# Performance work log

Measured on AMD Instinct MI355X. Metric: run time of the kernel, lower is better.

## Reference

```python
import jax, jax.numpy as jnp
import numpy as np


def setup_inputs() -> dict:
    key = jax.random.key(0)
    k1, k2, k3, k4 = jax.random.split(key, 4)
    N = 100000          # n_users + n_items nodes
    E = 1600000         # nonzeros in normalized adjacency (avg degree 16)
    D = 64              # embedding dim
    edge_row = jnp.sort(jax.random.randint(k1, (E,), 0, N, dtype=jnp.int32))
    edge_col = jax.random.randint(k2, (E,), 0, N, dtype=jnp.int32)
    edge_val = jax.random.uniform(k3, (E,), dtype=jnp.float32)
    embeds = jax.random.normal(k4, (N, D), dtype=jnp.float32)
    return {
        "edge_row": edge_row,
        "edge_col": edge_col,
        "edge_val": edge_val,
        "embeds": embeds,
        "num_nodes": N,
    }


def reference(edge_row, edge_col, edge_val, embeds, num_nodes):
    # out = A @ embeds, A given in COO: A[row[e], col[e]] = val[e]
    gathered = edge_val[:, None] * embeds[edge_col]        # [E, D]
    out = jax.ops.segment_sum(gathered, edge_row, num_segments=num_nodes)  # [N, D]
    return out
```

## Files before the change

### kernel.cpp

```cpp
#include <hip/hip_runtime.h>


#define GCN_D 64

typedef float f4 __attribute__((ext_vector_type(4)));
typedef unsigned int u32x2 __attribute__((ext_vector_type(2)));
typedef int i32x4 __attribute__((ext_vector_type(4)));
typedef float f32x4 __attribute__((ext_vector_type(4)));

__global__ __launch_bounds__(256) void prep_kernel(
    const float* __restrict__ embeds,
    unsigned char* __restrict__ ebq,
    float* __restrict__ scale,
    int quant_blocks,
    const int* __restrict__ edge_row, int* __restrict__ row_ptr, int E, int N)
{
    if ((int)blockIdx.x < quant_blocks) {
        const int t   = blockIdx.x * blockDim.x + threadIdx.x;
        const int row = t >> 3;
        if (row >= N) return;
        const int l8 = (threadIdx.x & 7) * 8;

        const f4 a = __builtin_nontemporal_load(
            (const f4*)(embeds + (size_t)row * GCN_D + l8));
        const f4 b = __builtin_nontemporal_load(
            (const f4*)(embeds + (size_t)row * GCN_D + l8 + 4));

        float m = fmaxf(fmaxf(fmaxf(fabsf(a.x), fabsf(a.y)),
                              fmaxf(fabsf(a.z), fabsf(a.w))),
                        fmaxf(fmaxf(fabsf(b.x), fabsf(b.y)),
                              fmaxf(fabsf(b.z), fabsf(b.w))));
        m = fmaxf(m, __shfl_xor(m, 1));
        m = fmaxf(m, __shfl_xor(m, 2));
        m = fmaxf(m, __shfl_xor(m, 4));

        const float inv = (m > 0.f) ? 127.f / m : 0.f;
        const int q0 = (int)rintf(fminf(fmaxf(a.x * inv, -127.f), 127.f)) + 128;
        const int q1 = (int)rintf(fminf(fmaxf(a.y * inv, -127.f), 127.f)) + 128;
        const int q2 = (int)rintf(fminf(fmaxf(a.z * inv, -127.f), 127.f)) + 128;
        const int q3 = (int)rintf(fminf(fmaxf(a.w * inv, -127.f), 127.f)) + 128;
        const int q4 = (int)rintf(fminf(fmaxf(b.x * inv, -127.f), 127.f)) + 128;
        const int q5 = (int)rintf(fminf(fmaxf(b.y * inv, -127.f), 127.f)) + 128;
        const int q6 = (int)rintf(fminf(fmaxf(b.z * inv, -127.f), 127.f)) + 128;
        const int q7 = (int)rintf(fminf(fmaxf(b.w * inv, -127.f), 127.f)) + 128;

        unsigned int p0 =
            (unsigned)q0 | ((unsigned)q1 << 8) | ((unsigned)q2 << 16) | ((unsigned)q3 << 24);
        unsigned int p1 =
            (unsigned)q4 | ((unsigned)q5 << 8) | ((unsigned)q6 << 16) | ((unsigned)q7 << 24);

        unsigned int* dst = (unsigned int*)(ebq + (size_t)row * GCN_D + l8);
        dst[0] = p0;
        dst[1] = p1;
        if ((threadIdx.x & 7) == 0) scale[row] = m * (1.f / 127.f);
    } else {
        const int e = (blockIdx.x - quant_blocks) * blockDim.x + threadIdx.x;
        if (e >= E) return;
        const int r    = edge_row[e];
        const int prev = (e == 0) ? -1 : edge_row[e - 1];
        for (int k = prev + 1; k <= r; ++k) row_ptr[k] = e;
        if (e == E - 1)
            for (int k = r + 1; k <= N; ++k) row_ptr[k] = E;
    }
}

__device__ __forceinline__ void q8_fma(unsigned int g, float w, f4& acc) {
    acc.x += w * (float)( g        & 0xffu);
    acc.y += w * (float)((g >> 8)  & 0xffu);
    acc.z += w * (float)((g >> 16) & 0xffu);
    acc.w += w * (float)( g >> 24);
}

__global__ __launch_bounds__(256) void gcn_row_q8_kernel(
    const int* __restrict__ row_ptr,
    const int* __restrict__ edge_col,
    const float* __restrict__ edge_val,
    const unsigned char* __restrict__ ebq,
    const float* __restrict__ scale,
    float* __restrict__ out,
    int N)
{
    const int tid = blockIdx.x * blockDim.x + threadIdx.x;
    const int row = tid >> 3;
    if (row >= N) return;
    const int db = (threadIdx.x & 7) * 8;

    const int p0 = row_ptr[row];
    const int p1 = row_ptr[row + 1];

    f4    acc0 = (f4)0.0f;
    f4    acc1 = (f4)0.0f;
    float wsum = 0.0f;
    int k = p0;

    while (k < p1 && (k & 3)) {
        const int c = edge_col[k];
        const u32x2 g = *(const u32x2*)(ebq + (size_t)c * GCN_D + db);
        const float w = edge_val[k] * scale[c];
        q8_fma(g.x, w, acc0);
        q8_fma(g.y, w, acc1);
        wsum += w;
        ++k;
    }

    for (; k + 7 < p1; k += 8) {
        const i32x4 ca = *(const i32x4*)(edge_col + k);
        const i32x4 cb = *(const i32x4*)(edge_col + k + 4);
        const f32x4 va = *(const f32x4*)(edge_val + k);
        const f32x4 vb = *(const f32x4*)(edge_val + k + 4);
        const int   c[8] = {ca.x, ca.y, ca.z, ca.w, cb.x, cb.y, cb.z, cb.w};
        const float v[8] = {va.x, va.y, va.z, va.w, vb.x, vb.y, vb.z, vb.w};
        u32x2 g[8];
        float s[8];
        #pragma unroll
        for (int j = 0; j < 8; ++j) {
            g[j] = *(const u32x2*)(ebq + (size_t)c[j] * GCN_D + db);
            s[j] = scale[c[j]];
        }
        #pragma unroll
        for (int j = 0; j < 8; ++j) {
            const float w = v[j] * s[j];
            q8_fma(g[j].x, w, acc0);
            q8_fma(g[j].y, w, acc1);
            wsum += w;
        }
    }

    if (k + 3 < p1) {
        const i32x4 ca = *(const i32x4*)(edge_col + k);
        const f32x4 va = *(const f32x4*)(edge_val + k);
        const int   c[4] = {ca.x, ca.y, ca.z, ca.w};
        const float v[4] = {va.x, va.y, va.z, va.w};
        u32x2 g[4];
        float s[4];
        #pragma unroll
        for (int j = 0; j < 4; ++j) {
            g[j] = *(const u32x2*)(ebq + (size_t)c[j] * GCN_D + db);
            s[j] = scale[c[j]];
        }
        #pragma unroll
        for (int j = 0; j < 4; ++j) {
            const float w = v[j] * s[j];
            q8_fma(g[j].x, w, acc0);
            q8_fma(g[j].y, w, acc1);
            wsum += w;
        }
        k += 4;
    }

    for (; k < p1; ++k) {
        const int c = edge_col[k];
        const u32x2 g = *(const u32x2*)(ebq + (size_t)c * GCN_D + db);
        const float w = edge_val[k] * scale[c];
        q8_fma(g.x, w, acc0);
        q8_fma(g.y, w, acc1);
        wsum += w;
    }

    const float z = 128.0f * wsum;
    acc0 = acc0 - z;
    acc1 = acc1 - z;

    __builtin_nontemporal_store(acc0, (f4*)(out + (size_t)row * GCN_D + db));
    __builtin_nontemporal_store(acc1, (f4*)(out + (size_t)row * GCN_D + db + 4));
}

extern "C" void kernel_launch(void* const* d_in, const int* in_sizes, int n_in,
                              void* d_out, int out_size, void* d_ws, size_t ws_size,
                              hipStream_t stream) {
    const int*   edge_row = (const int*)d_in[0];
    const int*   edge_col = (const int*)d_in[1];
    const float* edge_val = (const float*)d_in[2];
    const float* embeds   = (const float*)d_in[3];
    float*       out      = (float*)d_out;

    const int E = in_sizes[0];
    const int N = out_size / GCN_D;

    int* row_ptr = (int*)d_ws;
    const size_t sc_off = (((size_t)(N + 1) * 4) + 255) & ~(size_t)255;
    float* scale = (float*)((char*)d_ws + sc_off);
    const size_t q_off = ((sc_off + (size_t)N * 4) + 255) & ~(size_t)255;
    unsigned char* ebq = (unsigned char*)d_ws + q_off;

    const int quant_blocks = (N * 8 + 255) / 256;
    const int rp_blocks    = (E + 255) / 256;
    prep_kernel<<<quant_blocks + rp_blocks, 256, 0, stream>>>(
        embeds, ebq, scale, quant_blocks, edge_row, row_ptr, E, N);

    const int row_blocks = (N * 8 + 255) / 256;
    gcn_row_q8_kernel<<<row_blocks, 256, 0, stream>>>(
        row_ptr, edge_col, edge_val, ebq, scale, out, N);
}
```

Measured before the change: 127.6 us.

## Process two rows per 8-lane group with interleaved gathers

Each 8-lane group now handles two adjacent rows, interleaving 4-edge chunks from both rows so more independent gathers are in flight per thread. This replaces the aligned 8-wide vector loads of edge_col/edge_val with scalar loads in groups of 4 and adds a per-row drain loop. The grid is halved, which lowers total wave count but raises register use and adds load imbalance between the two rows.

```diff
diff --git a/kernel.cpp b/kernel.cpp
--- a/kernel.cpp
+++ b/kernel.cpp
@@ -5,8 +5,6 @@
 
 typedef float f4 __attribute__((ext_vector_type(4)));
 typedef unsigned int u32x2 __attribute__((ext_vector_type(2)));
-typedef int i32x4 __attribute__((ext_vector_type(4)));
-typedef float f32x4 __attribute__((ext_vector_type(4)));
 
 __global__ __launch_bounds__(256) void prep_kernel(
     const float* __restrict__ embeds,
@@ -71,6 +69,44 @@
     acc.w += w * (float)( g >> 24);
 }
 
+__device__ __forceinline__ void drain_row(
+    int k, int e, int db,
+    const int* __restrict__ edge_col,
+    const float* __restrict__ edge_val,
+    const unsigned char* __restrict__ ebq,
+    const float* __restrict__ scale,
+    f4& acc0, f4& acc1, float& wsum)
+{
+    for (; k + 3 < e; k += 4) {
+        int   c[4];
+        float v[4];
+        #pragma unroll
+        for (int j = 0; j < 4; ++j) { c[j] = edge_col[k + j]; v[j] = edge_val[k + j]; }
+        u32x2 g[4];
+        float s[4];
+        #pragma unroll
+        for (int j = 0; j < 4; ++j) {
+            g[j] = *(const u32x2*)(ebq + (size_t)c[j] * GCN_D + db);
+            s[j] = scale[c[j]];
+        }
+        #pragma unroll
+        for (int j = 0; j < 4; ++j) {
+            const float w = v[j] * s[j];
+            q8_fma(g[j].x, w, acc0);
+            q8_fma(g[j].y, w, acc1);
+            wsum += w;
+        }
+    }
+    for (; k < e; ++k) {
+        const int c = edge_col[k];
+        const u32x2 g = *(const u32x2*)(ebq + (size_t)c * GCN_D + db);
+        const float w = edge_val[k] * scale[c];
+        q8_fma(g.x, w, acc0);
+        q8_fma(g.y, w, acc1);
+        wsum += w;
+    }
+}
+
 __global__ __launch_bounds__(256) void gcn_row_q8_kernel(
     const int* __restrict__ row_ptr,
     const int* __restrict__ edge_col,
@@ -80,89 +116,76 @@
     float* __restrict__ out,
     int N)
 {
-    const int tid = blockIdx.x * blockDim.x + threadIdx.x;
-    const int row = tid >> 3;
-    if (row >= N) return;
+    const int tid  = blockIdx.x * blockDim.x + threadIdx.x;
+    const int pair = tid >> 3;
+    const int rowA = pair * 2;
+    if (rowA >= N) return;
     const int db = (threadIdx.x & 7) * 8;
 
-    const int p0 = row_ptr[row];
-    const int p1 = row_ptr[row + 1];
-
-    f4    acc0 = (f4)0.0f;
-    f4    acc1 = (f4)0.0f;
-    float wsum = 0.0f;
-    int k = p0;
-
-    while (k < p1 && (k & 3)) {
-        const int c = edge_col[k];
-        const u32x2 g = *(const u32x2*)(ebq + (size_t)c * GCN_D + db);
-        const float w = edge_val[k] * scale[c];
-        q8_fma(g.x, w, acc0);
-        q8_fma(g.y, w, acc1);
-        wsum += w;
-        ++k;
-    }
-
-    for (; k + 7 < p1; k += 8) {
-        const i32x4 ca = *(const i32x4*)(edge_col + k);
-        const i32x4 cb = *(const i32x4*)(edge_col + k + 4);
-        const f32x4 va = *(const f32x4*)(edge_val + k);
-        const f32x4 vb = *(const f32x4*)(edge_val + k + 4);
-        const int   c[8] = {ca.x, ca.y, ca.z, ca.w, cb.x, cb.y, cb.z, cb.w};
-        const float v[8] = {va.x, va.y, va.z, va.w, vb.x, vb.y, vb.z, vb.w};
-        u32x2 g[8];
-        float s[8];
-        #pragma unroll
-        for (int j = 0; j < 8; ++j) {
-            g[j] = *(const u32x2*)(ebq + (size_t)c[j] * GCN_D + db);
-            s[j] = scale[c[j]];
-        }
-        #pragma unroll
-        for (int j = 0; j < 8; ++j) {
-            const float w = v[j] * s[j];
-            q8_fma(g[j].x, w, acc0);
-            q8_fma(g[j].y, w, acc1);
-            wsum += w;
-        }
-    }
-
-    if (k + 3 < p1) {
-        const i32x4 ca = *(const i32x4*)(edge_col + k);
-        const f32x4 va = *(const f32x4*)(edge_val + k);
-        const int   c[4] = {ca.x, ca.y, ca.z, ca.w};
-        const float v[4] = {va.x, va.y, va.z, va.w};
-        u32x2 g[4];
-        float s[4];
-        #pragma unroll
-        for (int j = 0; j < 4; ++j) {
-            g[j] = *(const u32x2*)(ebq + (size_t)c[j] * GCN_D + db);
-            s[j] = scale[c[j]];
-        }
-        #pragma unroll
-        for (int j = 0; j < 4; ++j) {
-            const float w = v[j] * s[j];
-            q8_fma(g[j].x, w, acc0);
-            q8_fma(g[j].y, w, acc1);
-            wsum += w;
-        }
-        k += 4;
-    }
-
-    for (; k < p1; ++k) {
-        const int c = edge_col[k];
-        const u32x2 g = *(const u32x2*)(ebq + (size_t)c * GCN_D + db);
-        const float w = edge_val[k] * scale[c];
-        q8_fma(g.x, w, acc0);
-        q8_fma(g.y, w, acc1);
-        wsum += w;
-    }
-
-    const float z = 128.0f * wsum;
-    acc0 = acc0 - z;
-    acc1 = acc1 - z;
-
-    __builtin_nontemporal_store(acc0, (f4*)(out + (size_t)row * GCN_D + db));
-    __builtin_nontemporal_store(acc1, (f4*)(out + (size_t)row * GCN_D + db + 4));
+    const int  lo   = row_ptr[rowA];
+    const int  mid  = row_ptr[rowA + 1];
+    const bool hasB = (rowA + 1 < N);
+    const int  hi   = hasB ? row_ptr[rowA + 2] : mid;
+
+    f4    a0 = (f4)0.0f, a1 = (f4)0.0f;
+    f4    b0 = (f4)0.0f, b1 = (f4)0.0f;
+    float wsA = 0.0f, wsB = 0.0f;
+
+    int ka = lo, kb = mid;
+
+    while (ka + 3 < mid && kb + 3 < hi) {
+        int   cA[4], cB[4];
+        float vA[4], vB[4];
+        #pragma unroll
+        for (int j = 0; j < 4; ++j) { cA[j] = edge_col[ka + j]; vA[j] = edge_val[ka + j]; }
+        #pragma unroll
+        for (int j = 0; j < 4; ++j) { cB[j] = edge_col[kb + j]; vB[j] = edge_val[kb + j]; }
+        u32x2 gA[4], gB[4];
+        float sA[4], sB[4];
+        #pragma unroll
+        for (int j = 0; j < 4; ++j) {
+            gA[j] = *(const u32x2*)(ebq + (size_t)cA[j] * GCN_D + db);
+            sA[j] = scale[cA[j]];
+        }
+        #pragma unroll
+        for (int j = 0; j < 4; ++j) {
+            gB[j] = *(const u32x2*)(ebq + (size_t)cB[j] * GCN_D + db);
+            sB[j] = scale[cB[j]];
+        }
+        #pragma unroll
+        for (int j = 0; j < 4; ++j) {
+            const float w = vA[j] * sA[j];
+            q8_fma(gA[j].x, w, a0);
+            q8_fma(gA[j].y, w, a1);
+            wsA += w;
+        }
+        #pragma unroll
+        for (int j = 0; j < 4; ++j) {
+            const float w = vB[j] * sB[j];
+            q8_fma(gB[j].x, w, b0);
+            q8_fma(gB[j].y, w, b1);
+            wsB += w;
+        }
+        ka += 4;
+        kb += 4;
+    }
+
+    drain_row(ka, mid, db, edge_col, edge_val, ebq, scale, a0, a1, wsA);
+    drain_row(kb, hi,  db, edge_col, edge_val, ebq, scale, b0, b1, wsB);
+
+    const float zA = 128.0f * wsA;
+    a0 = a0 - zA;
+    a1 = a1 - zA;
+    __builtin_nontemporal_store(a0, (f4*)(out + (size_t)rowA * GCN_D + db));
+    __builtin_nontemporal_store(a1, (f4*)(out + (size_t)rowA * GCN_D + db + 4));
+
+    if (hasB) {
+        const float zB = 128.0f * wsB;
+        b0 = b0 - zB;
+        b1 = b1 - zB;
+        __builtin_nontemporal_store(b0, (f4*)(out + (size_t)(rowA + 1) * GCN_D + db));
+        __builtin_nontemporal_store(b1, (f4*)(out + (size_t)(rowA + 1) * GCN_D + db + 4));
+    }
 }
 
 extern "C" void kernel_launch(void* const* d_in, const int* in_sizes, int n_in,
@@ -188,7 +211,8 @@
     prep_kernel<<<quant_blocks + rp_blocks, 256, 0, stream>>>(
         embeds, ebq, scale, quant_blocks, edge_row, row_ptr, E, N);
 
-    const int row_blocks = (N * 8 + 255) / 256;
+    const int pairs      = (N + 1) / 2;
+    const int row_blocks = (pairs * 8 + 255) / 256;
     gcn_row_q8_kernel<<<row_blocks, 256, 0, stream>>>(
         row_ptr, edge_col, edge_val, ebq, scale, out, N);
 }
```

After: 135.9 us. 6.5% more time.
